# Optimization experiments

Measured on AMD Instinct MI355X. Metric: run time of the kernel, lower is better.

## Reference

```python
import jax, jax.numpy as jnp
import numpy as np

B, S, HID = 2, 2048, 4096
H, KVH, D = 32, 8, 128
THETA = 10000.0
SCALE = D ** -0.5


def _rope(x, positions):
    # x: [B, S, nH, D], positions: [B, S] int. Neox style: rotate halves.
    half = D // 2
    inv_freq = 1.0 / (THETA ** (jnp.arange(0, half, dtype=jnp.float32) / half))
    ang = positions.astype(jnp.float32)[..., None] * inv_freq  # [B,S,half]
    cos = jnp.cos(ang)[:, :, None, :]  # [B,S,1,half]
    sin = jnp.sin(ang)[:, :, None, :]
    x1, x2 = x[..., :half], x[..., half:]
    return jnp.concatenate([x1 * cos - x2 * sin, x2 * cos + x1 * sin], axis=-1)


def setup_inputs() -> dict:
    key = jax.random.key(0)
    k1, k2, k3, k4, k5 = jax.random.split(key, 5)
    std_in = HID ** -0.5
    return {
        "positions": jnp.tile(jnp.arange(S, dtype=jnp.int32), (B, 1)),
        "hidden_states": jax.random.normal(k1, (B, S, HID), jnp.float32),
        "wq": jax.random.normal(k2, (HID, H * D), jnp.float32) * std_in,
        "wk": jax.random.normal(k3, (HID, KVH * D), jnp.float32) * std_in,
        "wv": jax.random.normal(k4, (HID, KVH * D), jnp.float32) * std_in,
        "wo": jax.random.normal(k5, (H * D, HID), jnp.float32) * ((H * D) ** -0.5),
    }


def reference(positions, hidden_states, wq, wk, wv, wo):
    # Separate Q/K/V projections (bias=False)
    q = (hidden_states @ wq).reshape(B, S, H, D)
    k = (hidden_states @ wk).reshape(B, S, KVH, D)
    v = (hidden_states @ wv).reshape(B, S, KVH, D)
    # RoPE on q and k
    q = _rope(q, positions)
    k = _rope(k, positions)
    # GQA: expand KV heads to query heads
    group = H // KVH
    k = jnp.repeat(k, group, axis=2)  # [B,S,H,D]
    v = jnp.repeat(v, group, axis=2)
    # Causal scaled dot-product attention
    scores = jnp.einsum("bqhd,bkhd->bhqk", q, k) * SCALE
    causal = jnp.tril(jnp.ones((S, S), dtype=bool))
    scores = jnp.where(causal, scores, jnp.finfo(scores.dtype).min)
    probs = jax.nn.softmax(scores, axis=-1)
    attn = jnp.einsum("bhqk,bkhd->bqhd", probs, v).reshape(B, S, H * D)
    return attn @ wo
```

## Files before the change

### kernel.cpp

```cpp
#include <hip/hip_runtime.h>
#include <cstdint>

typedef __bf16 bf16;
typedef __attribute__((ext_vector_type(4))) __bf16 bf16x4;
typedef __attribute__((ext_vector_type(8))) __bf16 bf16x8;
typedef __attribute__((ext_vector_type(4))) float f32x4;

#define DEVI __device__ __forceinline__

#define BATCH 2
#define SEQ 2048
#define HID 4096
#define NH 32
#define NKVH 8
#define HD 128
#define QKVN 6144
#define MROWS 4096
#define ATT_SCALE 0.08838834764831845f
#define QSCALE (0.08838834764831845f * 1.4426950408889634f)

DEVI void gload_lds16(const bf16* g, bf16* l) {
  __builtin_amdgcn_global_load_lds(
      (__attribute__((address_space(1))) void*)(g),
      (__attribute__((address_space(3))) void*)(l), 16, 0, 0);
}

__global__ void h2b_kernel(const float* __restrict__ in, bf16* __restrict__ out) {
  long i = ((long)blockIdx.x * 256 + threadIdx.x) * 4;
  float4 v = *(const float4*)(in + i);
  bf16x4 o;
  o[0] = (bf16)v.x; o[1] = (bf16)v.y; o[2] = (bf16)v.z; o[3] = (bf16)v.w;
  *(bf16x4*)(out + i) = o;
}

__global__ void wtrans_kernel(const float* __restrict__ in, bf16* __restrict__ out,
                              int K, int N) {
  __shared__ float t[32][33];
  int n0 = blockIdx.x * 32, k0 = blockIdx.y * 32;
  int tx = threadIdx.x, ty = threadIdx.y;
#pragma unroll
  for (int r = 0; r < 4; ++r) {
    int k = ty + r * 8;
    t[k][tx] = in[(long)(k0 + k) * N + n0 + tx];
  }
  __syncthreads();
#pragma unroll
  for (int r = 0; r < 4; ++r) {
    int n = ty + r * 8;
    out[(long)(n0 + n) * K + k0 + tx] = (bf16)t[tx][n];
  }
}

__global__ void rope_kernel(bf16* __restrict__ qkv, const int* __restrict__ pos) {
  long t = (long)blockIdx.x * 256 + threadIdx.x;
  int d8 = (int)(t & 7) * 8;
  long u = t >> 3;
  int hh = (int)(u % 40);
  int row = (int)(u / 40);
  int colb = hh < NH ? hh * HD : NH * HD + (hh - NH) * HD;
  float p = (float)pos[row];
  bf16* base = qkv + (long)row * QKVN + colb + d8;
  bf16x8 x1v = *(const bf16x8*)(base);
  bf16x8 x2v = *(const bf16x8*)(base + 64);
  bf16x8 o1, o2;
#pragma unroll
  for (int j = 0; j < 8; ++j) {
    float inv_freq = exp2f((float)(d8 + j) * -0.2076205059304601f);
    float ang = p * inv_freq;
    float sn, cs;
    __sincosf(ang, &sn, &cs);
    float x1 = (float)x1v[j], x2 = (float)x2v[j];
    o1[j] = (bf16)(x1 * cs - x2 * sn);
    o2[j] = (bf16)(x2 * cs + x1 * sn);
  }
  *(bf16x8*)(base) = o1;
  *(bf16x8*)(base + 64) = o2;
}

__global__ void vtrans_kernel(const bf16* __restrict__ qkv, bf16* __restrict__ vt) {
  __shared__ bf16 t[32][33];
  int s0 = blockIdx.x * 32, d0 = blockIdx.y * 32, bk = blockIdx.z;
  int b = bk >> 3, kvh = bk & 7;
  int tx = threadIdx.x, ty = threadIdx.y;
#pragma unroll
  for (int r = 0; r < 4; ++r) {
    int s = ty + r * 8;
    t[s][tx] = qkv[(long)(b * SEQ + s0 + s) * QKVN + 5120 + kvh * HD + d0 + tx];
  }
  __syncthreads();
#pragma unroll
  for (int r = 0; r < 4; ++r) {
    int d = ty + r * 8;
    vt[((long)bk * HD + d0 + d) * SEQ + s0 + tx] = t[tx][d];
  }
}

template <typename OutT>
__global__ __launch_bounds__(512, 2)
void gemm256(const bf16* __restrict__ A, const bf16* __restrict__ BT,
             OutT* __restrict__ C, int M, int N, int K) {
  extern __shared__ __align__(16) bf16 lds[];
  const int tid = threadIdx.x;
  const int lane = tid & 63, wave = tid >> 6;
  const int wm = wave >> 1, wn = wave & 1;
  const int l16 = lane & 15, lhi = lane >> 4;
  const int nwg = gridDim.x * gridDim.y;
  const int bid = blockIdx.y * gridDim.x + blockIdx.x;
  const int cpx = nwg >> 3;
  const int swz = (bid & 7) * cpx + (bid >> 3);
  const int bx = swz % gridDim.x, by = swz / gridDim.x;
  const long bm0 = (long)by * 256, bn0 = (long)bx * 128;

  const int srow8 = lane >> 3;
  const int scol = (lane & 7) ^ srow8;

  const int NT = K >> 6;
  f32x4 acc[4][4] = {};

  auto stage = [&](int slot, int t) {
    const long k0 = (long)t << 6;
    bf16* dst = lds + slot * 24576;
#pragma unroll
    for (int i = 0; i < 4; ++i) {
      int r = (wave * 4 + i) * 8 + srow8;
      gload_lds16(A + (bm0 + r) * K + k0 + scol * 8,
                  dst + (wave * 4 + i) * 512 + lane * 8);
    }
#pragma unroll
    for (int i = 0; i < 2; ++i) {
      int r = (wave * 2 + i) * 8 + srow8;
      gload_lds16(BT + (bn0 + r) * K + k0 + scol * 8,
                  dst + 16384 + (wave * 2 + i) * 512 + lane * 8);
    }
  };

  stage(0, 0);
  stage(1, 1);

  for (int t = 0; t < NT; ++t) {
    asm volatile("s_waitcnt vmcnt(6)" ::: "memory");
    __builtin_amdgcn_s_barrier();
    __builtin_amdgcn_sched_barrier(0);
    const int nxt = (t + 2 < NT) ? t + 2 : NT - 1;
    stage((t + 2) % 3, nxt);
    const bf16* As = lds + (t % 3) * 24576;
    const bf16* Bs = As + 16384;
#pragma unroll
    for (int kk = 0; kk < 2; ++kk) {
      bf16x8 af[4], bw[4];
#pragma unroll
      for (int i = 0; i < 4; ++i) {
        int ar = wm * 64 + i * 16 + l16;
        af[i] = *(const bf16x8*)(As + ar * 64 + (((kk * 4 + lhi) ^ (ar & 7))) * 8);
        int br = wn * 64 + i * 16 + l16;
        bw[i] = *(const bf16x8*)(Bs + br * 64 + (((kk * 4 + lhi) ^ (br & 7))) * 8);
      }
      __builtin_amdgcn_s_setprio(1);
#pragma unroll
      for (int i = 0; i < 4; ++i)
#pragma unroll
        for (int j = 0; j < 4; ++j)
          acc[i][j] = __builtin_amdgcn_mfma_f32_16x16x32_bf16(af[i], bw[j], acc[i][j], 0, 0, 0);
      __builtin_amdgcn_s_setprio(0);
    }
  }
  asm volatile("s_waitcnt vmcnt(0)" ::: "memory");
#pragma unroll
  for (int i = 0; i < 4; ++i)
#pragma unroll
    for (int r = 0; r < 4; ++r) {
      long grow = bm0 + wm * 64 + i * 16 + lhi * 4 + r;
#pragma unroll
      for (int j = 0; j < 4; ++j) {
        long gcol = bn0 + wn * 64 + j * 16 + l16;
        C[grow * N + gcol] = (OutT)acc[i][j][r];
      }
    }
}

template <typename OutT>
__global__ __launch_bounds__(512, 2)
void gemm8p(const bf16* __restrict__ A, const bf16* __restrict__ BT,
            OutT* __restrict__ C, int M, int N, int K) {
  extern __shared__ __align__(16) bf16 lds[];
  const int tid = threadIdx.x;
  const int lane = tid & 63, wave = tid >> 6;
  const int wm = wave >> 2, wn = wave & 3;
  const int l16 = lane & 15, lhi = lane >> 4;
  const int nwg = gridDim.x * gridDim.y;
  const int bid = blockIdx.y * gridDim.x + blockIdx.x;
  const int cpx = nwg >> 3;
  const int swz = (bid & 7) * cpx + (bid >> 3);
  const int bx = swz % gridDim.x, by = swz / gridDim.x;
  const long bm0 = (long)by * 256, bn0 = (long)bx * 256;

  bf16* Alds = lds;
  bf16* Blds = lds + 32768;
  const int NT = K >> 6;

  f32x4 acc[8][4] = {};

  auto stageH = [&](const bf16* src, long row0, long k0, bf16* dst) {
#pragma unroll
    for (int j = 0; j < 2; ++j) {
      int r = j * 64 + (tid >> 3);
      int sc = (tid & 7) ^ (r & 7);
      gload_lds16(src + (row0 + r) * (long)K + k0 + sc * 8,
                  dst + j * 4096 + tid * 8);
    }
  };

  stageH(A, bm0, 0, Alds);
  stageH(A, bm0 + 128, 0, Alds + 8192);
  stageH(BT, bn0, 0, Blds);
  stageH(BT, bn0 + 128, 0, Blds + 8192);
  {
    long k1p = (NT > 1) ? 64 : 0;
    stageH(A, bm0, k1p, Alds + 16384);
    stageH(BT, bn0, k1p, Blds + 16384);
    stageH(BT, bn0 + 128, k1p, Blds + 24576);
  }
  asm volatile("s_waitcnt vmcnt(6)" ::: "memory");
  __builtin_amdgcn_s_barrier();

  const int arow0 = wm * 128 + l16;
  const int brow0 = wn * 64 + l16;

  for (int t = 0; t < NT; ++t) {
    const bf16* Ab = Alds + (t & 1) * 16384;
    const bf16* Bb = Blds + (t & 1) * 16384;
    bf16* Aopp = Alds + ((t + 1) & 1) * 16384;
    bf16* Asame = Alds + (t & 1) * 16384;
    bf16* Bsame = Blds + (t & 1) * 16384;
    const long k1 = (long)((t + 1 < NT) ? t + 1 : NT - 1) << 6;
    const long k2 = (long)((t + 2 < NT) ? t + 2 : NT - 1) << 6;

    bf16x8 a0[4][2], a1[4][2], b0[2][2], b1[2][2];
#pragma unroll
    for (int i = 0; i < 4; ++i) {
      int mr = arow0 + i * 16;
#pragma unroll
      for (int kk = 0; kk < 2; ++kk)
        a0[i][kk] = *(const bf16x8*)(Ab + mr * 64 + (((kk * 4 + lhi) ^ (mr & 7))) * 8);
    }
#pragma unroll
    for (int n = 0; n < 2; ++n) {
      int br = brow0 + n * 16;
#pragma unroll
      for (int kk = 0; kk < 2; ++kk)
        b0[n][kk] = *(const bf16x8*)(Bb + br * 64 + (((kk * 4 + lhi) ^ (br & 7))) * 8);
    }
    __builtin_amdgcn_s_barrier();
    asm volatile("s_waitcnt lgkmcnt(0)" ::: "memory");
    __builtin_amdgcn_sched_barrier(0);
    __builtin_amdgcn_s_setprio(1);
#pragma unroll
    for (int i = 0; i < 4; ++i)
#pragma unroll
      for (int n = 0; n < 2; ++n)
#pragma unroll
        for (int kk = 0; kk < 2; ++kk)
          acc[i][n] = __builtin_amdgcn_mfma_f32_16x16x32_bf16(a0[i][kk], b0[n][kk], acc[i][n], 0, 0, 0);
    __builtin_amdgcn_s_setprio(0);
    __builtin_amdgcn_s_barrier();
#pragma unroll
    for (int i = 0; i < 4; ++i) {
      int mr = arow0 + 64 + i * 16;
#pragma unroll
      for (int kk = 0; kk < 2; ++kk)
        a1[i][kk] = *(const bf16x8*)(Ab + mr * 64 + (((kk * 4 + lhi) ^ (mr & 7))) * 8);
    }
    stageH(A, bm0 + 128, k1, Aopp + 8192);
    __builtin_amdgcn_s_barrier();
    asm volatile("s_waitcnt lgkmcnt(0)" ::: "memory");
    __builtin_amdgcn_sched_barrier(0);
    __builtin_amdgcn_s_setprio(1);
#pragma unroll
    for (int i = 0; i < 4; ++i)
#pragma unroll
      for (int n = 0; n < 2; ++n)
#pragma unroll
        for (int kk = 0; kk < 2; ++kk)
          acc[4 + i][n] = __builtin_amdgcn_mfma_f32_16x16x32_bf16(a1[i][kk], b0[n][kk], acc[4 + i][n], 0, 0, 0);
    __builtin_amdgcn_s_setprio(0);
    __builtin_amdgcn_s_barrier();
#pragma unroll
    for (int n = 0; n < 2; ++n) {
      int br = brow0 + (n + 2) * 16;
#pragma unroll
      for (int kk = 0; kk < 2; ++kk)
        b1[n][kk] = *(const bf16x8*)(Bb + br * 64 + (((kk * 4 + lhi) ^ (br & 7))) * 8);
    }
    stageH(A, bm0, k2, Asame);
    __builtin_amdgcn_s_barrier();
    asm volatile("s_waitcnt lgkmcnt(0)" ::: "memory");
    __builtin_amdgcn_sched_barrier(0);
    __builtin_amdgcn_s_setprio(1);
#pragma unroll
    for (int i = 0; i < 4; ++i)
#pragma unroll
      for (int n = 0; n < 2; ++n)
#pragma unroll
        for (int kk = 0; kk < 2; ++kk)
          acc[4 + i][n + 2] = __builtin_amdgcn_mfma_f32_16x16x32_bf16(a1[i][kk], b1[n][kk], acc[4 + i][n + 2], 0, 0, 0);
    __builtin_amdgcn_s_setprio(0);
    __builtin_amdgcn_s_barrier();
    stageH(BT, bn0, k2, Bsame);
    stageH(BT, bn0 + 128, k2, Bsame + 8192);
    __builtin_amdgcn_s_barrier();
    __builtin_amdgcn_s_setprio(1);
#pragma unroll
    for (int i = 0; i < 4; ++i)
#pragma unroll
      for (int n = 0; n < 2; ++n)
#pragma unroll
        for (int kk = 0; kk < 2; ++kk)
          acc[i][n + 2] = __builtin_amdgcn_mfma_f32_16x16x32_bf16(a0[i][kk], b1[n][kk], acc[i][n + 2], 0, 0, 0);
    __builtin_amdgcn_s_setprio(0);
    asm volatile("s_waitcnt vmcnt(6)" ::: "memory");
    __builtin_amdgcn_s_barrier();
  }
  asm volatile("s_waitcnt vmcnt(0)" ::: "memory");
#pragma unroll
  for (int mi = 0; mi < 8; ++mi)
#pragma unroll
    for (int r = 0; r < 4; ++r) {
      long grow = bm0 + wm * 128 + mi * 16 + lhi * 4 + r;
#pragma unroll
      for (int n = 0; n < 4; ++n) {
        long gcol = bn0 + wn * 64 + n * 16 + l16;
        C[grow * N + gcol] = (OutT)acc[mi][n][r];
      }
    }
}

__global__ __launch_bounds__(512, 4)
void attn_kernel(const bf16* __restrict__ qkv, const bf16* __restrict__ vt,
                 bf16* __restrict__ out) {
  extern __shared__ __align__(16) bf16 smem[];
  const int pi = blockIdx.x, h = blockIdx.y, b = blockIdx.z;
  const int kvh = h >> 2;
  const int tid = threadIdx.x, lane = tid & 63, wave = tid >> 6;
  const int l16 = lane & 15, lhi = lane >> 4;
  const int kloc = lhi * 4;
  bf16* Pw = smem + 32768 + wave * 1024;

  const bf16* kpan = qkv + (long)(b * SEQ) * QKVN + 4096 + kvh * HD;
  const bf16* vpan = vt + (long)(b * NKVH + kvh) * HD * SEQ;

  auto stageKV = [&](int buf, int step) {
    const int kv0 = step * 64;
    bf16* kd = smem + buf * 8192;
    bf16* vd = smem + 16384 + buf * 8192;
#pragma unroll
    for (int i = 0; i < 2; ++i) {
      int kr = wave * 8 + i * 4 + lhi;
      gload_lds16(kpan + (long)(kv0 + kr) * QKVN + (l16 ^ (kr & 7)) * 8,
                  kd + (wave * 8 + i * 4) * 128);
      int vr = wave * 16 + i * 8 + (lane >> 3);
      gload_lds16(vpan + (long)vr * SEQ + kv0 + ((lane & 7) ^ (vr & 7)) * 8,
                  vd + (wave * 16 + i * 8) * 64);
    }
  };

  auto process_chunk = [&](int q0, int nsteps) {
    bf16x8 qf[4];
    const bf16* qb = qkv + (long)(b * SEQ + q0 + wave * 16 + l16) * QKVN + h * HD + lhi * 8;
#pragma unroll
    for (int di = 0; di < 4; ++di) {
      bf16x8 raw = *(const bf16x8*)(qb + di * 32);
      bf16x8 sc;
#pragma unroll
      for (int j = 0; j < 8; ++j) sc[j] = (bf16)((float)raw[j] * QSCALE);
      qf[di] = sc;
    }
    f32x4 oacc[8] = {};
    float m_run = -1e30f, l_run = 0.f;
    const int qg = q0 + wave * 16 + l16;

    stageKV(0, 0);
    __syncthreads();

    for (int step = 0; step < nsteps; ++step) {
      const int kv0 = step * 64;
      const int cur = step & 1;
      if (step + 1 < nsteps) stageKV(cur ^ 1, step + 1);
      const bf16* Kc = smem + cur * 8192;
      const bf16* Vc = smem + 16384 + cur * 8192;

      f32x4 s[4];
      __builtin_amdgcn_s_setprio(1);
#pragma unroll
      for (int c = 0; c < 4; ++c) {
        s[c] = (f32x4){0.f, 0.f, 0.f, 0.f};
        int kr = c * 16 + l16;
#pragma unroll
        for (int di = 0; di < 4; ++di) {
          bf16x8 kf = *(const bf16x8*)(Kc + kr * 128 + (((di * 4 + lhi) ^ (kr & 7))) * 8);
          s[c] = __builtin_amdgcn_mfma_f32_16x16x32_bf16(kf, qf[di], s[c], 0, 0, 0);
        }
      }
      __builtin_amdgcn_s_setprio(0);
#pragma unroll
      for (int c = 0; c < 4; ++c)
#pragma unroll
        for (int r = 0; r < 4; ++r) {
          int kcol = kv0 + c * 16 + kloc + r;
          if (kcol > qg) s[c][r] = -1e30f;
        }
      float mloc = s[0][0];
#pragma unroll
      for (int c = 0; c < 4; ++c)
#pragma unroll
        for (int r = 0; r < 4; ++r) mloc = fmaxf(mloc, s[c][r]);
      mloc = fmaxf(mloc, __shfl_xor(mloc, 16, 64));
      mloc = fmaxf(mloc, __shfl_xor(mloc, 32, 64));
      bool skip = __all(mloc - m_run <= 8.0f);
      float alpha = 1.f;
      if (!skip) {
        float mn = fmaxf(m_run, mloc);
        alpha = exp2f(m_run - mn);
        m_run = mn;
      }
      float sm = 0.f;
      bf16x4 pb[4];
#pragma unroll
      for (int c = 0; c < 4; ++c)
#pragma unroll
        for (int r = 0; r < 4; ++r) {
          float p = exp2f(s[c][r] - m_run);
          sm += p;
          pb[c][r] = (bf16)p;
        }
      sm += __shfl_xor(sm, 16, 64);
      sm += __shfl_xor(sm, 32, 64);
      l_run = l_run * alpha + sm;
#pragma unroll
      for (int c = 0; c < 4; ++c) {
        int sl = (c * 2 + (lhi >> 1)) ^ (l16 & 7);
        *(bf16x4*)(Pw + l16 * 64 + sl * 8 + (lhi & 1) * 4) = pb[c];
      }
      if (!skip) {
        float a_o[4];
#pragma unroll
        for (int r = 0; r < 4; ++r) a_o[r] = __shfl(alpha, kloc + r, 64);
#pragma unroll
        for (int dj = 0; dj < 8; ++dj)
#pragma unroll
          for (int r = 0; r < 4; ++r) oacc[dj][r] *= a_o[r];
      }
      __builtin_amdgcn_s_setprio(1);
#pragma unroll
      for (int kh = 0; kh < 2; ++kh) {
        bf16x8 pf = *(const bf16x8*)(Pw + l16 * 64 + (((kh * 4 + lhi) ^ (l16 & 7))) * 8);
#pragma unroll
        for (int dj = 0; dj < 8; ++dj) {
          int vr = dj * 16 + l16;
          bf16x8 vf = *(const bf16x8*)(Vc + vr * 64 + (((kh * 4 + lhi) ^ (vr & 7))) * 8);
          oacc[dj] = __builtin_amdgcn_mfma_f32_16x16x32_bf16(pf, vf, oacc[dj], 0, 0, 0);
        }
      }
      __builtin_amdgcn_s_setprio(0);
      __syncthreads();
    }
    float linv[4];
#pragma unroll
    for (int r = 0; r < 4; ++r) linv[r] = 1.f / __shfl(l_run, kloc + r, 64);
#pragma unroll
    for (int r = 0; r < 4; ++r) {
      long orow = (long)(b * SEQ + q0 + wave * 16 + lhi * 4 + r);
#pragma unroll
      for (int dj = 0; dj < 8; ++dj)
        out[orow * (NH * HD) + h * HD + dj * 16 + l16] = (bf16)(oacc[dj][r] * linv[r]);
    }
  };

  process_chunk(pi * 128, 2 * pi + 2);
  process_chunk((15 - pi) * 128, 32 - 2 * pi);
}

extern "C" void kernel_launch(void* const* d_in, const int* in_sizes, int n_in,
                              void* d_out, int out_size, void* d_ws, size_t ws_size,
                              hipStream_t stream) {
  const int* positions = (const int*)d_in[0];
  const float* hidden = (const float*)d_in[1];
  const float* wq = (const float*)d_in[2];
  const float* wk = (const float*)d_in[3];
  const float* wv = (const float*)d_in[4];
  const float* wo = (const float*)d_in[5];
  float* out = (float*)d_out;
  char* ws = (char*)d_ws;

  const size_t SZ_H = (size_t)MROWS * HID * 2;
  const size_t SZ_WQKV = (size_t)QKVN * HID * 2;
  const size_t SZ_WO = (size_t)HID * HID * 2;
  bf16* h_bf = (bf16*)(ws);
  bf16* wqkvT = (bf16*)(ws + SZ_H);
  bf16* woT = (bf16*)(ws + SZ_H + SZ_WQKV);
  bf16* qkv = (bf16*)(ws + SZ_H + SZ_WQKV + SZ_WO);
  bf16* attn = h_bf;
  bf16* vtbuf = wqkvT;

  const int G8P_SMEM = 131072;
  const int R3_SMEM = 3 * 24576 * 2;
  const int ATTN_SMEM = 40960 * 2;
  auto* g1 = gemm256<bf16>;
  auto* g2 = gemm8p<float>;
  hipFuncSetAttribute(reinterpret_cast<const void*>(g1),
                      hipFuncAttributeMaxDynamicSharedMemorySize, R3_SMEM);
  hipFuncSetAttribute(reinterpret_cast<const void*>(g2),
                      hipFuncAttributeMaxDynamicSharedMemorySize, G8P_SMEM);
  hipFuncSetAttribute(reinterpret_cast<const void*>(attn_kernel),
                      hipFuncAttributeMaxDynamicSharedMemorySize, ATTN_SMEM);

  h2b_kernel<<<(MROWS * (long)HID) / (256 * 4), 256, 0, stream>>>(hidden, h_bf);
  dim3 t32(32, 8);
  wtrans_kernel<<<dim3(HID / 32, HID / 32), t32, 0, stream>>>(wq, wqkvT, HID, HID);
  wtrans_kernel<<<dim3(1024 / 32, HID / 32), t32, 0, stream>>>(wk, wqkvT + (long)4096 * HID, HID, 1024);
  wtrans_kernel<<<dim3(1024 / 32, HID / 32), t32, 0, stream>>>(wv, wqkvT + (long)5120 * HID, HID, 1024);
  wtrans_kernel<<<dim3(HID / 32, HID / 32), t32, 0, stream>>>(wo, woT, HID, HID);
  gemm256<bf16><<<dim3(QKVN / 128, MROWS / 256), 512, R3_SMEM, stream>>>(h_bf, wqkvT, qkv, MROWS, QKVN, HID);
  rope_kernel<<<(MROWS * 40 * 8) / 256, 256, 0, stream>>>(qkv, positions);
  vtrans_kernel<<<dim3(SEQ / 32, HD / 32, BATCH * NKVH), t32, 0, stream>>>(qkv, vtbuf);
  attn_kernel<<<dim3(8, NH, BATCH), 512, ATTN_SMEM, stream>>>(qkv, vtbuf, attn);
  gemm8p<float><<<dim3(HID / 256, MROWS / 256), 512, G8P_SMEM, stream>>>(attn, woT, out, MROWS, HID, HID);
}
```

Measured before the change: 528.3 us.

## Fuse Q RoPE into attention, vectorize weight transpose, skip unneeded causal masking

Result: faster. 508.6 us (-3.7%).

```diff
diff --git a/kernel.cpp b/kernel.cpp
--- a/kernel.cpp
+++ b/kernel.cpp
@@ -18,6 +18,7 @@
 #define MROWS 4096
 #define ATT_SCALE 0.08838834764831845f
 #define QSCALE (0.08838834764831845f * 1.4426950408889634f)
+#define ROPE_C (-0.2076205059304601f)
 
 DEVI void gload_lds16(const bf16* g, bf16* l) {
   __builtin_amdgcn_global_load_lds(
@@ -35,38 +36,43 @@
 
 __global__ void wtrans_kernel(const float* __restrict__ in, bf16* __restrict__ out,
                               int K, int N) {
-  __shared__ float t[32][33];
-  int n0 = blockIdx.x * 32, k0 = blockIdx.y * 32;
-  int tx = threadIdx.x, ty = threadIdx.y;
-#pragma unroll
-  for (int r = 0; r < 4; ++r) {
-    int k = ty + r * 8;
-    t[k][tx] = in[(long)(k0 + k) * N + n0 + tx];
+  __shared__ float t[64][65];
+  int n0 = blockIdx.x * 64, k0 = blockIdx.y * 64;
+  int tid = threadIdx.x;
+  int tx = tid & 15, ty = tid >> 4;
+#pragma unroll
+  for (int rr = 0; rr < 4; ++rr) {
+    int k = ty * 4 + rr;
+    float4 v = *(const float4*)(in + (long)(k0 + k) * N + n0 + tx * 4);
+    t[k][tx * 4 + 0] = v.x; t[k][tx * 4 + 1] = v.y;
+    t[k][tx * 4 + 2] = v.z; t[k][tx * 4 + 3] = v.w;
   }
   __syncthreads();
-#pragma unroll
-  for (int r = 0; r < 4; ++r) {
-    int n = ty + r * 8;
-    out[(long)(n0 + n) * K + k0 + tx] = (bf16)t[tx][n];
-  }
-}
-
-__global__ void rope_kernel(bf16* __restrict__ qkv, const int* __restrict__ pos) {
+  int kc = tid & 7, nn = tid >> 3;
+#pragma unroll
+  for (int pp = 0; pp < 2; ++pp) {
+    int n = nn + pp * 32;
+    bf16x8 o;
+#pragma unroll
+    for (int j = 0; j < 8; ++j) o[j] = (bf16)t[kc * 8 + j][n];
+    *(bf16x8*)(out + (long)(n0 + n) * K + k0 + kc * 8) = o;
+  }
+}
+
+__global__ void ropek_kernel(bf16* __restrict__ qkv, const int* __restrict__ pos) {
   long t = (long)blockIdx.x * 256 + threadIdx.x;
   int d8 = (int)(t & 7) * 8;
   long u = t >> 3;
-  int hh = (int)(u % 40);
-  int row = (int)(u / 40);
-  int colb = hh < NH ? hh * HD : NH * HD + (hh - NH) * HD;
+  int hh = (int)(u % 8);
+  int row = (int)(u / 8);
   float p = (float)pos[row];
-  bf16* base = qkv + (long)row * QKVN + colb + d8;
+  bf16* base = qkv + (long)row * QKVN + 4096 + hh * HD + d8;
   bf16x8 x1v = *(const bf16x8*)(base);
   bf16x8 x2v = *(const bf16x8*)(base + 64);
   bf16x8 o1, o2;
 #pragma unroll
   for (int j = 0; j < 8; ++j) {
-    float inv_freq = exp2f((float)(d8 + j) * -0.2076205059304601f);
-    float ang = p * inv_freq;
+    float ang = p * exp2f((float)(d8 + j) * ROPE_C);
     float sn, cs;
     __sincosf(ang, &sn, &cs);
     float x1 = (float)x1v[j], x2 = (float)x2v[j];
@@ -336,7 +342,7 @@
 
 __global__ __launch_bounds__(512, 4)
 void attn_kernel(const bf16* __restrict__ qkv, const bf16* __restrict__ vt,
-                 bf16* __restrict__ out) {
+                 const int* __restrict__ pos, bf16* __restrict__ out) {
   extern __shared__ __align__(16) bf16 smem[];
   const int pi = blockIdx.x, h = blockIdx.y, b = blockIdx.z;
   const int kvh = h >> 2;
@@ -364,19 +370,30 @@
   };
 
   auto process_chunk = [&](int q0, int nsteps) {
+    const int qrow = q0 + wave * 16 + l16;
+    float p = (float)pos[b * SEQ + qrow];
+    const bf16* qb = qkv + (long)(b * SEQ + qrow) * QKVN + h * HD + lhi * 8;
+    bf16x8 raw[4];
+#pragma unroll
+    for (int di = 0; di < 4; ++di) raw[di] = *(const bf16x8*)(qb + di * 32);
     bf16x8 qf[4];
-    const bf16* qb = qkv + (long)(b * SEQ + q0 + wave * 16 + l16) * QKVN + h * HD + lhi * 8;
-#pragma unroll
-    for (int di = 0; di < 4; ++di) {
-      bf16x8 raw = *(const bf16x8*)(qb + di * 32);
-      bf16x8 sc;
-#pragma unroll
-      for (int j = 0; j < 8; ++j) sc[j] = (bf16)((float)raw[j] * QSCALE);
-      qf[di] = sc;
-    }
+#pragma unroll
+    for (int pr = 0; pr < 2; ++pr)
+#pragma unroll
+      for (int j = 0; j < 8; ++j) {
+        int d = lhi * 8 + pr * 32 + j;
+        float ang = p * exp2f((float)d * ROPE_C);
+        float sn, cs;
+        __sincosf(ang, &sn, &cs);
+        float x1 = (float)raw[pr][j], x2 = (float)raw[pr + 2][j];
+        qf[pr][j] = (bf16)((x1 * cs - x2 * sn) * QSCALE);
+        qf[pr + 2][j] = (bf16)((x2 * cs + x1 * sn) * QSCALE);
+      }
+
     f32x4 oacc[8] = {};
     float m_run = -1e30f, l_run = 0.f;
-    const int qg = q0 + wave * 16 + l16;
+    const int qg = qrow;
+    const int qwmin = q0 + wave * 16;
 
     stageKV(0, 0);
     __syncthreads();
@@ -401,13 +418,15 @@
         }
       }
       __builtin_amdgcn_s_setprio(0);
-#pragma unroll
-      for (int c = 0; c < 4; ++c)
-#pragma unroll
-        for (int r = 0; r < 4; ++r) {
-          int kcol = kv0 + c * 16 + kloc + r;
-          if (kcol > qg) s[c][r] = -1e30f;
-        }
+      if (kv0 + 63 > qwmin) {
+#pragma unroll
+        for (int c = 0; c < 4; ++c)
+#pragma unroll
+          for (int r = 0; r < 4; ++r) {
+            int kcol = kv0 + c * 16 + kloc + r;
+            if (kcol > qg) s[c][r] = -1e30f;
+          }
+      }
       float mloc = s[0][0];
 #pragma unroll
       for (int c = 0; c < 4; ++c)
@@ -428,9 +447,9 @@
       for (int c = 0; c < 4; ++c)
 #pragma unroll
         for (int r = 0; r < 4; ++r) {
-          float p = exp2f(s[c][r] - m_run);
-          sm += p;
-          pb[c][r] = (bf16)p;
+          float pv = exp2f(s[c][r] - m_run);
+          sm += pv;
+          pb[c][r] = (bf16)pv;
         }
       sm += __shfl_xor(sm, 16, 64);
       sm += __shfl_xor(sm, 32, 64);
@@ -514,14 +533,14 @@
                       hipFuncAttributeMaxDynamicSharedMemorySize, ATTN_SMEM);
 
   h2b_kernel<<<(MROWS * (long)HID) / (256 * 4), 256, 0, stream>>>(hidden, h_bf);
+  wtrans_kernel<<<dim3(HID / 64, HID / 64), 256, 0, stream>>>(wq, wqkvT, HID, HID);
+  wtrans_kernel<<<dim3(1024 / 64, HID / 64), 256, 0, stream>>>(wk, wqkvT + (long)4096 * HID, HID, 1024);
+  wtrans_kernel<<<dim3(1024 / 64, HID / 64), 256, 0, stream>>>(wv, wqkvT + (long)5120 * HID, HID, 1024);
+  wtrans_kernel<<<dim3(HID / 64, HID / 64), 256, 0, stream>>>(wo, woT, HID, HID);
+  gemm256<bf16><<<dim3(QKVN / 128, MROWS / 256), 512, R3_SMEM, stream>>>(h_bf, wqkvT, qkv, MROWS, QKVN, HID);
+  ropek_kernel<<<(MROWS * 8 * 8) / 256, 256, 0, stream>>>(qkv, positions);
   dim3 t32(32, 8);
-  wtrans_kernel<<<dim3(HID / 32, HID / 32), t32, 0, stream>>>(wq, wqkvT, HID, HID);
-  wtrans_kernel<<<dim3(1024 / 32, HID / 32), t32, 0, stream>>>(wk, wqkvT + (long)4096 * HID, HID, 1024);
-  wtrans_kernel<<<dim3(1024 / 32, HID / 32), t32, 0, stream>>>(wv, wqkvT + (long)5120 * HID, HID, 1024);
-  wtrans_kernel<<<dim3(HID / 32, HID / 32), t32, 0, stream>>>(wo, woT, HID, HID);
-  gemm256<bf16><<<dim3(QKVN / 128, MROWS / 256), 512, R3_SMEM, stream>>>(h_bf, wqkvT, qkv, MROWS, QKVN, HID);
-  rope_kernel<<<(MROWS * 40 * 8) / 256, 256, 0, stream>>>(qkv, positions);
   vtrans_kernel<<<dim3(SEQ / 32, HD / 32, BATCH * NKVH), t32, 0, stream>>>(qkv, vtbuf);
-  attn_kernel<<<dim3(8, NH, BATCH), 512, ATTN_SMEM, stream>>>(qkv, vtbuf, attn);
+  attn_kernel<<<dim3(8, NH, BATCH), 512, ATTN_SMEM, stream>>>(qkv, vtbuf, positions, attn);
   gemm8p<float><<<dim3(HID / 256, MROWS / 256), 512, G8P_SMEM, stream>>>(attn, woT, out, MROWS, HID, HID);
 }
```
